# Kernel optimization log

Measured on AMD Instinct MI355X. Metric: run time of the kernel, lower is better.

The kernel has to match this reference:

```python
import jax, jax.numpy as jnp
import numpy as np
from jax import lax

KS = 3  # kernel_size


def setup_inputs() -> dict:
    key = jax.random.key(0)
    k1, k2, k3 = jax.random.split(key, 3)
    B, D, C_IN, F = 4, 96, 16, 16
    feat = jax.random.normal(k1, (B, D, D, D, C_IN), dtype=jnp.float32)
    index = jax.random.randint(k2, (B, D, D, D), 0, 2, dtype=jnp.int32)
    # glorot-style scale for w [c_in * ks^3, filters]
    fan_in = C_IN * KS ** 3
    w = jax.random.normal(k3, (fan_in, F), dtype=jnp.float32) * jnp.float32(np.sqrt(2.0 / (fan_in + F)))
    b = jnp.zeros((F,), dtype=jnp.float32)
    return {"feat": feat, "index": index, "w": w, "b": b}


def reference(feat, index, w, b):
    # SparseConv: for every voxel where index != 0, gather the ks^3 neighborhood
    # (out-of-bounds neighbors read as zero), flatten to [N, ks^3 * C_in],
    # matmul with w, add b, and scatter back (zeros elsewhere).
    # The meshgrid('ij') offset order followed by reshape([-1, ks^3 * C_in])
    # makes w row index = ((dx*ks + dy)*ks + dz)*C_in + c_in, i.e. exactly a
    # dense 3-D cross-correlation kernel w.reshape(ks, ks, ks, C_in, F) with
    # SAME zero padding; the scatter_nd equals masking the output by index != 0.
    c_in = feat.shape[-1]
    filters = w.shape[-1]
    w_conv = w.reshape(KS, KS, KS, c_in, filters)  # DHWIO
    out = lax.conv_general_dilated(
        feat, w_conv,
        window_strides=(1, 1, 1),
        padding="SAME",
        dimension_numbers=("NDHWC", "DHWIO", "NDHWC"),
    ) + b
    mask = (index != 0)[..., None]  # [B, X, Y, Z, 1]
    return jnp.where(mask, out, jnp.zeros((), dtype=out.dtype))
```

## Files before the change

### kernel.cpp

```cpp
#include <hip/hip_runtime.h>

#define DSZ 96
#define CIN 16
#define NF  16
#define NXT (DSZ / 8)
#define NYT (DSZ / 8)
#define NZT (DSZ / 16)

typedef __attribute__((ext_vector_type(8))) short short8;
typedef __attribute__((ext_vector_type(4))) float f32x4;

union I4S8 { int4 i; short8 s; };

__global__ void pack_w(const float* __restrict__ w, short* __restrict__ wpack) {
  const int t = threadIdx.x >> 6;
  const int l = threadIdx.x & 63;
  const int tap = 2 * t + (l >> 5);
  const int cib = ((l >> 4) & 1) * 8;
  const int f = l & 15;
  short v[8];
#pragma unroll
  for (int j = 0; j < 8; ++j) {
    float x = (tap <= 26) ? w[(tap * 16 + cib + j) * 16 + f] : 0.0f;
    unsigned u = __float_as_uint(x);
    u = (u + 0x7FFFu + ((u >> 16) & 1u)) >> 16;
    v[j] = (short)u;
  }
  short8 s;
#pragma unroll
  for (int j = 0; j < 8; ++j) s[j] = v[j];
  reinterpret_cast<short8*>(wpack)[t * 64 + l] = s;
}

__device__ __forceinline__ int lds_byte(int col, int zp, int h16) {
  int byte = col * 576 + zp * 32 + h16;
  return byte ^ ((zp & 4) << 2);
}

__global__ __launch_bounds__(512, 4) void conv_mfma_lds(
    const float* __restrict__ feat, const int* __restrict__ index,
    const float* __restrict__ bias, const short8* __restrict__ wpack,
    float* __restrict__ out) {
  __shared__ short smem[100 * 18 * 16];

  const int tid = threadIdx.x;
  const int lane = tid & 63;
  const int wid = tid >> 6;

  const int d = blockIdx.x;
  int L = (d & 7) * (gridDim.x >> 3) + (d >> 3);
  const int yt = L % NYT;  L /= NYT;
  const int zt = L % NZT;  L /= NZT;
  const int xt = L % NXT;
  const int b  = L / NXT;
  const int x0 = xt * 8, y0 = yt * 8, z0 = zt * 16;

  short8 bw[14];
#pragma unroll
  for (int t = 0; t < 14; ++t) bw[t] = wpack[t * 64 + lane];

  for (int it = tid; it < 1800; it += 512) {
    const int col = it / 18;
    const int zp  = it - col * 18;
    const int colx = col / 10;
    const int coly = col - colx * 10;
    const int gx = x0 + colx - 1, gy = y0 + coly - 1, gz = z0 + zp - 1;
    const bool ok = ((unsigned)gx < (unsigned)DSZ) &
                    ((unsigned)gy < (unsigned)DSZ) &
                    ((unsigned)gz < (unsigned)DSZ);
    const long off = ok ? ((long)(((b * DSZ + gx) * DSZ + gy) * DSZ + gz) * CIN) : 0;
    const float4* p = reinterpret_cast<const float4*>(feat + off);
    float4 q0 = p[0], q1 = p[1], q2 = p[2], q3 = p[3];
    unsigned m0 = __builtin_amdgcn_perm(__float_as_uint(q0.y), __float_as_uint(q0.x), 0x07060302u);
    unsigned m1 = __builtin_amdgcn_perm(__float_as_uint(q0.w), __float_as_uint(q0.z), 0x07060302u);
    unsigned m2 = __builtin_amdgcn_perm(__float_as_uint(q1.y), __float_as_uint(q1.x), 0x07060302u);
    unsigned m3 = __builtin_amdgcn_perm(__float_as_uint(q1.w), __float_as_uint(q1.z), 0x07060302u);
    unsigned m4 = __builtin_amdgcn_perm(__float_as_uint(q2.y), __float_as_uint(q2.x), 0x07060302u);
    unsigned m5 = __builtin_amdgcn_perm(__float_as_uint(q2.w), __float_as_uint(q2.z), 0x07060302u);
    unsigned m6 = __builtin_amdgcn_perm(__float_as_uint(q3.y), __float_as_uint(q3.x), 0x07060302u);
    unsigned m7 = __builtin_amdgcn_perm(__float_as_uint(q3.w), __float_as_uint(q3.z), 0x07060302u);
    if (!ok) { m0 = m1 = m2 = m3 = m4 = m5 = m6 = m7 = 0u; }
    *reinterpret_cast<int4*>((char*)smem + lds_byte(col, zp, 0)) =
        make_int4(m0, m1, m2, m3);
    *reinterpret_cast<int4*>((char*)smem + lds_byte(col, zp, 16)) =
        make_int4(m4, m5, m6, m7);
  }
  __syncthreads();

  const int z   = lane & 15;
  const int h16 = lane & 16;
  const int tp  = lane >> 5;
  const int fq  = lane & 15;
  const int hq  = lane >> 4;
  const float bf = bias[fq];
  const int cx = wid;

#pragma unroll 1
  for (int cy = 0; cy < 8; ++cy) {
    int cb[9];
#pragma unroll
    for (int dd = 0; dd < 9; ++dd) {
      const int dx = dd / 3, dy = dd - 3 * (dd / 3);
      cb[dd] = ((cx + dx) * 10 + (cy + dy)) * 576;
    }
    f32x4 acc0 = {0.f, 0.f, 0.f, 0.f};
    f32x4 acc1 = {0.f, 0.f, 0.f, 0.f};
#pragma unroll
    for (int t = 0; t < 14; ++t) {
      const int tapA = 2 * t;
      const int tapB = (2 * t + 1 <= 26) ? (2 * t + 1) : 26;
      const int dA = (tapA / 9) * 3 + (tapA / 3) % 3;
      const int dB = (tapB / 9) * 3 + (tapB / 3) % 3;
      const int dzA = tapA % 3, dzB = tapB % 3;
      const int base = tp ? cb[dB] : cb[dA];
      const int zz = z + (tp ? dzB : dzA);
      const int byte = (base + zz * 32 + h16) ^ ((zz & 4) << 2);
      I4S8 u;
      u.i = *reinterpret_cast<const int4*>((const char*)smem + byte);
      if (t & 1)
        acc1 = __builtin_amdgcn_mfma_f32_16x16x32_bf16(u.s, bw[t], acc1, 0, 0, 0);
      else
        acc0 = __builtin_amdgcn_mfma_f32_16x16x32_bf16(u.s, bw[t], acc0, 0, 0, 0);
    }
    const int gx = x0 + cx, gy = y0 + cy;
    const int vbase = ((b * DSZ + gx) * DSZ + gy) * DSZ + z0;
    const int4 iv = *reinterpret_cast<const int4*>(index + vbase + hq * 4);
    const int ir0 = iv.x, ir1 = iv.y, ir2 = iv.z, ir3 = iv.w;
    float* op = out + (long)(vbase + hq * 4) * NF + fq;
    op[0 * NF] = ir0 ? (acc0[0] + acc1[0] + bf) : 0.0f;
    op[1 * NF] = ir1 ? (acc0[1] + acc1[1] + bf) : 0.0f;
    op[2 * NF] = ir2 ? (acc0[2] + acc1[2] + bf) : 0.0f;
    op[3 * NF] = ir3 ? (acc0[3] + acc1[3] + bf) : 0.0f;
  }
}

__global__ __launch_bounds__(256) void sparse_conv_f32(
    const float* __restrict__ feat, const int* __restrict__ index,
    const float* __restrict__ w, const float* __restrict__ bias,
    float* __restrict__ out) {
  const int v = blockIdx.x * 256 + threadIdx.x;
  const int z = v % DSZ;
  int t = v / DSZ;
  const int y = t % DSZ; t /= DSZ;
  const int x = t % DSZ;
  const int bb = t / DSZ;
  float acc[NF];
#pragma unroll
  for (int f = 0; f < NF; ++f) acc[f] = bias[f];
  const bool active = (index[v] != 0);
#pragma unroll 1
  for (int kx = -1; kx <= 1; ++kx) {
    const int xx = x + kx;
    const bool okx = ((unsigned)xx < (unsigned)DSZ);
#pragma unroll 1
    for (int ky = -1; ky <= 1; ++ky) {
      const int yy = y + ky;
      const bool oky = okx && ((unsigned)yy < (unsigned)DSZ);
#pragma unroll 1
      for (int kz = -1; kz <= 1; ++kz) {
        const int zz = z + kz;
        const bool ok = oky && ((unsigned)zz < (unsigned)DSZ);
        const long long off = ((((long long)bb * DSZ + xx) * DSZ + yy) * DSZ + zz) * CIN;
        float4 q0, q1, q2, q3;
        if (ok) {
          const float4* fp = reinterpret_cast<const float4*>(feat + off);
          q0 = fp[0]; q1 = fp[1]; q2 = fp[2]; q3 = fp[3];
        } else {
          q0 = q1 = q2 = q3 = make_float4(0.f, 0.f, 0.f, 0.f);
        }
        const float fv[CIN] = {q0.x, q0.y, q0.z, q0.w, q1.x, q1.y, q1.z, q1.w,
                               q2.x, q2.y, q2.z, q2.w, q3.x, q3.y, q3.z, q3.w};
        const float* wr = w + ((((kx + 1) * 3 + (ky + 1)) * 3 + (kz + 1)) * CIN) * NF;
#pragma unroll
        for (int ci = 0; ci < CIN; ++ci) {
          const float fvv = fv[ci];
#pragma unroll
          for (int f = 0; f < NF; ++f) acc[f] = fmaf(fvv, wr[ci * NF + f], acc[f]);
        }
      }
    }
  }
  float4* op = reinterpret_cast<float4*>(out + (long long)v * NF);
  if (active) {
    op[0] = make_float4(acc[0], acc[1], acc[2], acc[3]);
    op[1] = make_float4(acc[4], acc[5], acc[6], acc[7]);
    op[2] = make_float4(acc[8], acc[9], acc[10], acc[11]);
    op[3] = make_float4(acc[12], acc[13], acc[14], acc[15]);
  } else {
    const float4 z4 = make_float4(0.f, 0.f, 0.f, 0.f);
    op[0] = z4; op[1] = z4; op[2] = z4; op[3] = z4;
  }
}

extern "C" void kernel_launch(void* const* d_in, const int* in_sizes, int n_in,
                              void* d_out, int out_size, void* d_ws, size_t ws_size,
                              hipStream_t stream) {
  const float* feat  = (const float*)d_in[0];
  const int*   index = (const int*)d_in[1];
  const float* w     = (const float*)d_in[2];
  const float* bias  = (const float*)d_in[3];
  float*       out   = (float*)d_out;

  const int nvox = in_sizes[1];

  if (ws_size < 14 * 64 * 8 * sizeof(short)) {
    sparse_conv_f32<<<nvox / 256, 256, 0, stream>>>(feat, index, w, bias, out);
    return;
  }

  short* wpack = (short*)d_ws;
  pack_w<<<1, 14 * 64, 0, stream>>>(w, wpack);

  const int blocks = 4 * NXT * NYT * NZT;
  conv_mfma_lds<<<blocks, 512, 0, stream>>>(feat, index, bias,
                                            (const short8*)wpack, out);
}
```

Before: 139.5 us.

## Pipeline z-slab staging with MFMA compute in persistent 1024-thread blocks

Each block now covers three consecutive 16-deep z slabs instead of one and uses 1024 threads, with 16 waves splitting the y rows. The global loads for the next slab are issued into registers before computing the current slab, then written to LDS after a barrier. LDS addresses are also precomputed per lane. The goal is to hide global load latency behind MFMA work and to amortize weight loads. The cost is more registers, extra barriers, and fewer blocks (1152), which may lower occupancy.

```diff
diff --git a/kernel.cpp b/kernel.cpp
--- a/kernel.cpp
+++ b/kernel.cpp
@@ -3,9 +3,6 @@
 #define DSZ 96
 #define CIN 16
 #define NF  16
-#define NXT (DSZ / 8)
-#define NYT (DSZ / 8)
-#define NZT (DSZ / 16)
 
 typedef __attribute__((ext_vector_type(8))) short short8;
 typedef __attribute__((ext_vector_type(4))) float f32x4;
@@ -32,106 +29,141 @@
   reinterpret_cast<short8*>(wpack)[t * 64 + l] = s;
 }
 
-__device__ __forceinline__ int lds_byte(int col, int zp, int h16) {
-  int byte = col * 576 + zp * 32 + h16;
-  return byte ^ ((zp & 4) << 2);
-}
-
-__global__ __launch_bounds__(512, 4) void conv_mfma_lds(
+__global__ __launch_bounds__(1024, 4) void conv_mfma_pipe(
     const float* __restrict__ feat, const int* __restrict__ index,
     const float* __restrict__ bias, const short8* __restrict__ wpack,
     float* __restrict__ out) {
   __shared__ short smem[100 * 18 * 16];
 
-  const int tid = threadIdx.x;
+  const int tid  = threadIdx.x;
   const int lane = tid & 63;
-  const int wid = tid >> 6;
+  const int wid  = tid >> 6;
 
   const int d = blockIdx.x;
-  int L = (d & 7) * (gridDim.x >> 3) + (d >> 3);
-  const int yt = L % NYT;  L /= NYT;
-  const int zt = L % NZT;  L /= NZT;
-  const int xt = L % NXT;
-  const int b  = L / NXT;
-  const int x0 = xt * 8, y0 = yt * 8, z0 = zt * 16;
+  int L = (d & 7) * 144 + (d >> 3);
+  const int yt = L % 12;  L /= 12;
+  const int xt = L % 12;  L /= 12;
+  const int zb = L & 1;
+  const int b  = L >> 1;
+  const int x0 = xt * 8, y0 = yt * 8, zbase = zb * 48;
 
   short8 bw[14];
 #pragma unroll
   for (int t = 0; t < 14; ++t) bw[t] = wpack[t * 64 + lane];
 
-  for (int it = tid; it < 1800; it += 512) {
-    const int col = it / 18;
-    const int zp  = it - col * 18;
-    const int colx = col / 10;
-    const int coly = col - colx * 10;
-    const int gx = x0 + colx - 1, gy = y0 + coly - 1, gz = z0 + zp - 1;
-    const bool ok = ((unsigned)gx < (unsigned)DSZ) &
-                    ((unsigned)gy < (unsigned)DSZ) &
-                    ((unsigned)gz < (unsigned)DSZ);
-    const long off = ok ? ((long)(((b * DSZ + gx) * DSZ + gy) * DSZ + gz) * CIN) : 0;
-    const float4* p = reinterpret_cast<const float4*>(feat + off);
-    float4 q0 = p[0], q1 = p[1], q2 = p[2], q3 = p[3];
-    unsigned m0 = __builtin_amdgcn_perm(__float_as_uint(q0.y), __float_as_uint(q0.x), 0x07060302u);
-    unsigned m1 = __builtin_amdgcn_perm(__float_as_uint(q0.w), __float_as_uint(q0.z), 0x07060302u);
-    unsigned m2 = __builtin_amdgcn_perm(__float_as_uint(q1.y), __float_as_uint(q1.x), 0x07060302u);
-    unsigned m3 = __builtin_amdgcn_perm(__float_as_uint(q1.w), __float_as_uint(q1.z), 0x07060302u);
-    unsigned m4 = __builtin_amdgcn_perm(__float_as_uint(q2.y), __float_as_uint(q2.x), 0x07060302u);
-    unsigned m5 = __builtin_amdgcn_perm(__float_as_uint(q2.w), __float_as_uint(q2.z), 0x07060302u);
-    unsigned m6 = __builtin_amdgcn_perm(__float_as_uint(q3.y), __float_as_uint(q3.x), 0x07060302u);
-    unsigned m7 = __builtin_amdgcn_perm(__float_as_uint(q3.w), __float_as_uint(q3.z), 0x07060302u);
-    if (!ok) { m0 = m1 = m2 = m3 = m4 = m5 = m6 = m7 = 0u; }
-    *reinterpret_cast<int4*>((char*)smem + lds_byte(col, zp, 0)) =
-        make_int4(m0, m1, m2, m3);
-    *reinterpret_cast<int4*>((char*)smem + lds_byte(col, zp, 16)) =
-        make_int4(m4, m5, m6, m7);
-  }
-  __syncthreads();
-
-  const int z   = lane & 15;
-  const int h16 = lane & 16;
-  const int tp  = lane >> 5;
-  const int fq  = lane & 15;
-  const int hq  = lane >> 4;
+  const int cx = wid & 7, cyh = wid >> 3;
+  const int wbase = (cx * 10 + cyh * 4) * 576;
+  int pre[3];
+#pragma unroll
+  for (int dz = 0; dz < 3; ++dz) {
+    const int zp = (lane & 15) + dz;
+    pre[dz] = (zp * 32 + (lane & 16)) ^ ((zp & 4) << 2);
+  }
+  int laddr[14];
+#pragma unroll
+  for (int t = 0; t < 14; ++t) {
+    const int tapA = 2 * t;
+    const int tapB = (2 * t + 1 <= 26) ? (2 * t + 1) : 26;
+    const int cA = ((tapA / 9) * 10 + (tapA / 3) % 3) * 576;
+    const int cB = ((tapB / 9) * 10 + (tapB / 3) % 3) * 576;
+    const int aA = cA + pre[tapA % 3];
+    const int aB = cB + pre[tapB % 3];
+    laddr[t] = ((lane >> 5) ? aB : aA) + wbase;
+  }
+
+  const int fq = lane & 15, hq = lane >> 4;
   const float bf = bias[fq];
-  const int cx = wid;
-
-#pragma unroll 1
-  for (int cy = 0; cy < 8; ++cy) {
-    int cb[9];
-#pragma unroll
-    for (int dd = 0; dd < 9; ++dd) {
-      const int dx = dd / 3, dy = dd - 3 * (dd / 3);
-      cb[dd] = ((cx + dx) * 10 + (cy + dy)) * 576;
-    }
-    f32x4 acc0 = {0.f, 0.f, 0.f, 0.f};
-    f32x4 acc1 = {0.f, 0.f, 0.f, 0.f};
-#pragma unroll
-    for (int t = 0; t < 14; ++t) {
-      const int tapA = 2 * t;
-      const int tapB = (2 * t + 1 <= 26) ? (2 * t + 1) : 26;
-      const int dA = (tapA / 9) * 3 + (tapA / 3) % 3;
-      const int dB = (tapB / 9) * 3 + (tapB / 3) % 3;
-      const int dzA = tapA % 3, dzB = tapB % 3;
-      const int base = tp ? cb[dB] : cb[dA];
-      const int zz = z + (tp ? dzB : dzA);
-      const int byte = (base + zz * 32 + h16) ^ ((zz & 4) << 2);
-      I4S8 u;
-      u.i = *reinterpret_cast<const int4*>((const char*)smem + byte);
-      if (t & 1)
-        acc1 = __builtin_amdgcn_mfma_f32_16x16x32_bf16(u.s, bw[t], acc1, 0, 0, 0);
-      else
-        acc0 = __builtin_amdgcn_mfma_f32_16x16x32_bf16(u.s, bw[t], acc0, 0, 0, 0);
-    }
-    const int gx = x0 + cx, gy = y0 + cy;
-    const int vbase = ((b * DSZ + gx) * DSZ + gy) * DSZ + z0;
-    const int4 iv = *reinterpret_cast<const int4*>(index + vbase + hq * 4);
-    const int ir0 = iv.x, ir1 = iv.y, ir2 = iv.z, ir3 = iv.w;
-    float* op = out + (long)(vbase + hq * 4) * NF + fq;
-    op[0 * NF] = ir0 ? (acc0[0] + acc1[0] + bf) : 0.0f;
-    op[1 * NF] = ir1 ? (acc0[1] + acc1[1] + bf) : 0.0f;
-    op[2 * NF] = ir2 ? (acc0[2] + acc1[2] + bf) : 0.0f;
-    op[3 * NF] = ir3 ? (acc0[3] + acc1[3] + bf) : 0.0f;
-  }
+  const char* smb = (const char*)smem;
+
+  float4 sf[4][2];
+  int    sok[4];
+
+  auto stage_issue = [&](int z0) {
+#pragma unroll
+    for (int k = 0; k < 4; ++k) {
+      const int i = tid + k * 1024;
+      const int col = i / 36;
+      const int r = i - col * 36;
+      const int zp = r >> 1, g = r & 1;
+      const int colx = col / 10, coly = col - colx * 10;
+      const int gx = x0 + colx - 1, gy = y0 + coly - 1, gz = z0 - 1 + zp;
+      const bool ok = (i < 3600) & ((unsigned)gx < (unsigned)DSZ) &
+                      ((unsigned)gy < (unsigned)DSZ) &
+                      ((unsigned)gz < (unsigned)DSZ);
+      const long off =
+          ok ? ((long)(((b * DSZ + gx) * DSZ + gy) * DSZ + gz) * CIN + g * 8) : 0;
+      const float4* p = reinterpret_cast<const float4*>(feat + off);
+      sf[k][0] = p[0];
+      sf[k][1] = p[1];
+      sok[k] = ok;
+    }
+  };
+
+  auto stage_write = [&]() {
+#pragma unroll
+    for (int k = 0; k < 4; ++k) {
+      const int i = tid + k * 1024;
+      if (i < 3600) {
+        const int col = i / 36;
+        const int r = i - col * 36;
+        const int zp = r >> 1, g = r & 1;
+        unsigned m0 = __builtin_amdgcn_perm(__float_as_uint(sf[k][0].y),
+                                            __float_as_uint(sf[k][0].x), 0x07060302u);
+        unsigned m1 = __builtin_amdgcn_perm(__float_as_uint(sf[k][0].w),
+                                            __float_as_uint(sf[k][0].z), 0x07060302u);
+        unsigned m2 = __builtin_amdgcn_perm(__float_as_uint(sf[k][1].y),
+                                            __float_as_uint(sf[k][1].x), 0x07060302u);
+        unsigned m3 = __builtin_amdgcn_perm(__float_as_uint(sf[k][1].w),
+                                            __float_as_uint(sf[k][1].z), 0x07060302u);
+        if (!sok[k]) { m0 = 0u; m1 = 0u; m2 = 0u; m3 = 0u; }
+        const int byte = (col * 576 + zp * 32 + g * 16) ^ ((zp & 4) << 2);
+        *reinterpret_cast<int4*>((char*)smem + byte) = make_int4(m0, m1, m2, m3);
+      }
+    }
+  };
+
+  auto compute = [&](int z0) {
+#pragma unroll
+    for (int j = 0; j < 4; ++j) {
+      f32x4 acc0 = {0.f, 0.f, 0.f, 0.f};
+      f32x4 acc1 = {0.f, 0.f, 0.f, 0.f};
+#pragma unroll
+      for (int t = 0; t < 14; ++t) {
+        I4S8 u;
+        u.i = *reinterpret_cast<const int4*>(smb + laddr[t] + j * 576);
+        if (t & 1)
+          acc1 = __builtin_amdgcn_mfma_f32_16x16x32_bf16(u.s, bw[t], acc1, 0, 0, 0);
+        else
+          acc0 = __builtin_amdgcn_mfma_f32_16x16x32_bf16(u.s, bw[t], acc0, 0, 0, 0);
+      }
+      const int gy = y0 + cyh * 4 + j;
+      const int vbase = ((b * DSZ + (x0 + cx)) * DSZ + gy) * DSZ + z0;
+      const int4 iv = *reinterpret_cast<const int4*>(index + vbase + hq * 4);
+      float* op = out + (long)(vbase + hq * 4) * NF + fq;
+      op[0 * NF] = iv.x ? (acc0[0] + acc1[0] + bf) : 0.0f;
+      op[1 * NF] = iv.y ? (acc0[1] + acc1[1] + bf) : 0.0f;
+      op[2 * NF] = iv.z ? (acc0[2] + acc1[2] + bf) : 0.0f;
+      op[3 * NF] = iv.w ? (acc0[3] + acc1[3] + bf) : 0.0f;
+    }
+  };
+
+  stage_issue(zbase);
+  stage_write();
+  __syncthreads();
+
+  stage_issue(zbase + 16);
+  compute(zbase);
+  __syncthreads();
+  stage_write();
+  __syncthreads();
+
+  stage_issue(zbase + 32);
+  compute(zbase + 16);
+  __syncthreads();
+  stage_write();
+  __syncthreads();
+
+  compute(zbase + 32);
 }
 
 __global__ __launch_bounds__(256) void sparse_conv_f32(
@@ -211,7 +243,7 @@
   short* wpack = (short*)d_ws;
   pack_w<<<1, 14 * 64, 0, stream>>>(w, wpack);
 
-  const int blocks = 4 * NXT * NYT * NZT;
-  conv_mfma_lds<<<blocks, 512, 0, stream>>>(feat, index, bias,
-                                            (const short8*)wpack, out);
-}
+  const int blocks = 4 * 2 * 12 * 12;
+  conv_mfma_pipe<<<blocks, 1024, 0, stream>>>(feat, index, bias,
+                                              (const short8*)wpack, out);
+}
```

Result: slower. 165.2 us (+18.4%).
